# Optimization experiments

Measured on AMD Instinct MI355X. Metric: run time of the kernel, lower is better.

The kernel has to match this reference:

```python
import jax, jax.numpy as jnp
import numpy as np
from math import factorial

B, C, D = 1024, 10, 16
EPS = 1e-07


def _moment_weights(dim, order):
    # weight[idx] = prod(multiplicity!)/order!  (de-duplicates symmetric index tuples)
    if order == 1:
        return np.ones((dim,), dtype=np.float32)
    grids = np.meshgrid(*([np.arange(dim)] * order), indexing='ij')
    idx = np.stack(grids, axis=-1)  # [dim]*order + [order]
    prodm = np.ones(idx.shape[:-1], dtype=np.float64)
    for p in range(order):
        r = np.ones(idx.shape[:-1], dtype=np.float64)
        for q in range(p):
            r += (idx[..., q] == idx[..., p])
        prodm *= r  # running multiplicities multiply to prod(m!)
    return (prodm / float(factorial(order))).astype(np.float32)


def _gauss_moments(dim, order):
    # joint moments of N(0, I) via Isserlis' theorem
    eye = np.eye(dim)
    if order == 1:
        return np.zeros((dim,), np.float32)
    if order == 2:
        return eye.astype(np.float32)
    if order == 3:
        return np.zeros((dim, dim, dim), np.float32)
    g = (np.einsum('ij,kl->ijkl', eye, eye)
         + np.einsum('ik,jl->ijkl', eye, eye)
         + np.einsum('il,jk->ijkl', eye, eye))
    return g.astype(np.float32)


def _sroot(x, c1, p, c2):
    # signed compressive root: sign(sign(x)+0.1) * ((|x|+c1)^p - c2)
    return jnp.sign(jnp.sign(x) + 0.1) * (jnp.power(jnp.abs(x) + c1, p) - c2)


def setup_inputs() -> dict:
    key = jax.random.key(0)
    k1, k2, k3 = jax.random.split(key, 3)
    return {
        'embedding': jax.random.normal(k1, (B, D), dtype=jnp.float32),
        'centers': jax.random.normal(k2, (C, D), dtype=jnp.float32),
        'logits': jax.random.normal(k3, (B, C), dtype=jnp.float32),
        'gm1': jnp.asarray(_gauss_moments(D, 1)),
        'gm2': jnp.asarray(_gauss_moments(D, 2)),
        'gm3': jnp.asarray(_gauss_moments(D, 3)),
        'gm4': jnp.asarray(_gauss_moments(D, 4)),
        'mw1': jnp.asarray(_moment_weights(D, 1)),
        'mw2': jnp.asarray(_moment_weights(D, 2)),
        'mw3': jnp.asarray(_moment_weights(D, 3)),
        'mw4': jnp.asarray(_moment_weights(D, 4)),
    }


def reference(embedding, centers, logits, gm1, gm2, gm3, gm4, mw1, mw2, mw3, mw4):
    num_classes = logits.shape[1]
    assign = jnp.argmax(logits, axis=-1)                      # [B]
    onehot = jax.nn.one_hot(assign, num_classes, dtype=embedding.dtype)  # [B,C]
    diff = embedding[:, None, :] - centers[None, :, :]        # [B,C,D]
    d = diff * onehot[:, :, None]                             # diff_onehot [B,C,D]
    cw = jnp.sum(onehot, axis=0)                              # cluster_weight [C]

    # fused moment contractions (original materializes [B,C,D^k] then sums over B;
    # onehot is 0/1 so onehot^k == onehot -> identical math)
    m1 = jnp.sum(d, axis=0) / (cw[:, None] + EPS)                             # [C,D]
    m2 = jnp.einsum('bci,bcj->cij', d, d) / (cw[:, None, None] + EPS)         # [C,D,D]
    m3 = jnp.einsum('bci,bcj,bck->cijk', d, d, d)                             # [C,D,D,D] (no count division, as in original)
    m4 = jnp.einsum('bci,bcj,bck,bcl->cijkl', d, d, d, d)                     # [C,D,D,D,D]

    m2 = _sroot(m2, 0.25, 0.5, 0.5)
    m3 = _sroot(m3, 0.19245008973, 0.3333333333, 0.57735026919)
    m4 = _sroot(m4, 0.15749013123, 0.25, 0.62996052494)
    t1 = gm1
    t2 = _sroot(gm2, 0.25, 0.5, 0.5)
    t3 = _sroot(gm3, 0.19245008973, 0.3333333333, 0.57735026919)
    t4 = _sroot(gm4, 0.15749013123, 0.25, 0.62996052494)

    cwn = cw / jnp.sum(cw)                                     # [C]
    w1 = cwn[:, None] * mw1[None, :]
    w2 = cwn[:, None, None] * mw2[None]
    w3 = cwn[:, None, None, None] * mw3[None]
    w4 = cwn[:, None, None, None, None] * mw4[None]

    p1 = jnp.sum(w1 * jnp.square(m1 - t1[None]))
    p2 = jnp.sum(w2 * jnp.square(m2 - t2[None]))
    p3 = jnp.sum(w3 * jnp.square(m3 - t3[None]))
    p4 = jnp.sum(w4 * jnp.square(m4 - t4[None]))
    return 1.0 * p1 + 0.5 * p2 + 0.25 * p3 + 0.125 * p4
```

## Files before the change

### kernel.cpp

```cpp
#include <hip/hip_runtime.h>
#include <math.h>

#define BN 1024
#define CN 10
#define DN 16
#define NE1 16
#define NE2 136
#define NE3 816
#define NE4 3876
#define NENT 4844
#define EB 19
#define CH 256
#define EPSV 1e-7f

__device__ __forceinline__ int H2f(int n){ return n*(n+1)/2; }
__device__ __forceinline__ int H3f(int n){ return n*(n+1)*(n+2)/6; }

__device__ __forceinline__ float sroot2f(float x){
  float s = (x<0.f)?-1.f:1.f;
  return s*(sqrtf(fabsf(x)+0.25f)-0.5f);
}
__device__ __forceinline__ float sroot3f(float x){
  float s=(x<0.f)?-1.f:1.f;
  return s*(cbrtf(fabsf(x)+0.19245008973f)-0.57735026919f);
}
__device__ __forceinline__ float sroot4f(float x){
  float s=(x<0.f)?-1.f:1.f;
  return s*(sqrtf(sqrtf(fabsf(x)+0.15749013123f))-0.62996052494f);
}

__global__ __launch_bounds__(1024) void ka(
    const float* __restrict__ logits,
    int* __restrict__ counts, int* __restrict__ idxlist,
    float* __restrict__ acc, int* __restrict__ ticket) {
  int tid  = threadIdx.x;
  int lane = tid & 63;
  int wave = tid >> 6;
  if (tid == 0) { acc[0] = 0.f; ticket[0] = 0; }

  const float* lr = logits + tid*CN;
  float best = lr[0]; int bi = 0;
  #pragma unroll
  for (int c=1;c<CN;c++){ float v=lr[c]; if (v>best){best=v;bi=c;} }

  __shared__ int wcnt[16][CN];
  int lanerank = 0;
  #pragma unroll
  for (int c=0;c<CN;c++){
    unsigned long long m = __ballot(bi==c);
    if (bi==c) lanerank = __popcll(m & ((1ull<<lane)-1ull));
    if (lane==0) wcnt[wave][c] = __popcll(m);
  }
  __syncthreads();
  int off = 0;
  for (int w=0; w<wave; w++) off += wcnt[w][bi];
  idxlist[bi*BN + off + lanerank] = tid;

  if (tid < CN) {
    int t = 0;
    #pragma unroll
    for (int w=0; w<16; w++) t += wcnt[w][tid];
    counts[tid] = t;
  }
}

__global__ __launch_bounds__(256) void kb(
    const float* __restrict__ emb, const float* __restrict__ centers,
    const float* __restrict__ gm1, const float* __restrict__ gm2,
    const float* __restrict__ gm3, const float* __restrict__ gm4,
    const int* __restrict__ counts, const int* __restrict__ idxlist,
    float* __restrict__ acc, int* __restrict__ ticket,
    float* __restrict__ out) {
  __shared__ float sx[17][CH+1];
  __shared__ float red[256];
  int tid = threadIdx.x;
  int c  = blockIdx.x / EB;
  int eb = blockIdx.x % EB;
  int cnt = counts[c];

  for (int n=tid; n<CH+1; n+=256) sx[16][n] = 1.f;

  int e = eb*256 + tid;
  int ii=16, jj=16, kk=16, ll=16, order=1;
  float tg = 0.f;
  bool valid = (e < NENT);
  if (valid) {
    if (e < NE1) {
      order=1; ii=e;
      tg = gm1[ii];
    } else if (e < NE1+NE2) {
      order=2; int r = e-NE1;
      int i=0; while (r >= DN-i){ r -= DN-i; i++; }
      ii=i; jj=i+r;
      tg = sroot2f(gm2[ii*DN+jj]);
    } else if (e < NE1+NE2+NE3) {
      order=3; int r = e-(NE1+NE2);
      int i=0; while (r >= H2f(DN-i)){ r -= H2f(DN-i); i++; }
      int j=i; while (r >= DN-j){ r -= DN-j; j++; }
      ii=i; jj=j; kk=j+r;
      tg = sroot3f(gm3[(ii*DN+jj)*DN+kk]);
    } else {
      order=4; int r = e-(NE1+NE2+NE3);
      int i=0; while (r >= H3f(DN-i)){ r -= H3f(DN-i); i++; }
      int j=i; while (r >= H2f(DN-j)){ r -= H2f(DN-j); j++; }
      int k=j; while (r >= DN-k){ r -= DN-k; k++; }
      ii=i; jj=j; kk=k; ll=k+r;
      tg = sroot4f(gm4[((ii*DN+jj)*DN+kk)*DN+ll]);
    }
  }

  float mom = 0.f;
  for (int base=0; base<cnt; base+=CH) {
    int m = min(CH, cnt-base);
    __syncthreads();
    if (tid < m) {
      int b = idxlist[c*BN + base + tid];
      const float4* er = (const float4*)(emb + b*DN);
      const float4* cr = (const float4*)(centers + c*DN);
      float4 e0=er[0], e1=er[1], e2=er[2], e3=er[3];
      float4 c0=cr[0], c1=cr[1], c2=cr[2], c3=cr[3];
      float v[16];
      v[0]=e0.x-c0.x; v[1]=e0.y-c0.y; v[2]=e0.z-c0.z; v[3]=e0.w-c0.w;
      v[4]=e1.x-c1.x; v[5]=e1.y-c1.y; v[6]=e1.z-c1.z; v[7]=e1.w-c1.w;
      v[8]=e2.x-c2.x; v[9]=e2.y-c2.y; v[10]=e2.z-c2.z; v[11]=e2.w-c2.w;
      v[12]=e3.x-c3.x; v[13]=e3.y-c3.y; v[14]=e3.z-c3.z; v[15]=e3.w-c3.w;
      #pragma unroll
      for (int i=0;i<16;i++) sx[i][tid] = v[i];
    }
    __syncthreads();
    for (int n=0; n<m; n++) {
      mom += sx[ii][n]*sx[jj][n]*sx[kk][n]*sx[ll][n];
    }
  }

  float contrib = 0.f;
  if (valid) {
    float mval = mom;
    if (order <= 2) mval /= ((float)cnt + EPSV);
    float v;
    if      (order==1) v = mval - tg;
    else if (order==2) v = sroot2f(mval) - tg;
    else if (order==3) v = sroot3f(mval) - tg;
    else               v = sroot4f(mval) - tg;
    float lw = (order==1)?1.f:(order==2)?0.5f:(order==3)?0.25f:0.125f;
    float cwn = (float)cnt * (1.f/1024.f);
    contrib = lw * cwn * v * v;
  }

  red[tid] = contrib;
  __syncthreads();
  for (int s=128; s>0; s>>=1) {
    if (tid < s) red[tid] += red[tid+s];
    __syncthreads();
  }
  if (tid==0) {
    atomicAdd(acc, red[0]);
    __threadfence();
    int old = atomicAdd(ticket, 1);
    if (old == (int)gridDim.x - 1) {
      float total = atomicAdd(acc, 0.0f);
      out[0] = total;
    }
  }
}

extern "C" void kernel_launch(void* const* d_in, const int* in_sizes, int n_in,
                              void* d_out, int out_size, void* d_ws, size_t ws_size,
                              hipStream_t stream) {
  const float* emb  = (const float*)d_in[0];
  const float* cen  = (const float*)d_in[1];
  const float* logi = (const float*)d_in[2];
  const float* gm1  = (const float*)d_in[3];
  const float* gm2  = (const float*)d_in[4];
  const float* gm3  = (const float*)d_in[5];
  const float* gm4  = (const float*)d_in[6];

  int*   counts  = (int*)d_ws;
  int*   idxlist = counts + CN;
  float* acc     = (float*)(idxlist + CN*BN);
  int*   ticket  = (int*)(acc + 1);

  ka<<<1, 1024, 0, stream>>>(logi, counts, idxlist, acc, ticket);
  kb<<<CN*EB, 256, 0, stream>>>(emb, cen, gm1, gm2, gm3, gm4,
                                counts, idxlist, acc, ticket, (float*)d_out);
}
```

Measured before the change: 20.59 us.

## Fuse argmax bucketing into moment kernel and drop ticket-based final reduction

```diff
diff --git a/kernel.cpp b/kernel.cpp
--- a/kernel.cpp
+++ b/kernel.cpp
@@ -29,56 +29,45 @@
   return s*(sqrtf(sqrtf(fabsf(x)+0.15749013123f))-0.62996052494f);
 }
 
-__global__ __launch_bounds__(1024) void ka(
+__global__ __launch_bounds__(256) void kb(
+    const float* __restrict__ emb, const float* __restrict__ centers,
     const float* __restrict__ logits,
-    int* __restrict__ counts, int* __restrict__ idxlist,
-    float* __restrict__ acc, int* __restrict__ ticket) {
+    const float* __restrict__ gm1, const float* __restrict__ gm2,
+    const float* __restrict__ gm3, const float* __restrict__ gm4,
+    float* __restrict__ out) {
+  __shared__ float sx[17][CH+1];
+  __shared__ float red[256];
+  __shared__ int   memb[BN];
+  __shared__ int   wcnt[4][4];
   int tid  = threadIdx.x;
   int lane = tid & 63;
   int wave = tid >> 6;
-  if (tid == 0) { acc[0] = 0.f; ticket[0] = 0; }
+  int c  = blockIdx.x / EB;
+  int eb = blockIdx.x % EB;
 
-  const float* lr = logits + tid*CN;
-  float best = lr[0]; int bi = 0;
+  for (int n=tid; n<CH+1; n+=256) sx[16][n] = 1.f;
+
+  int rank_r[4]; bool match_r[4];
   #pragma unroll
-  for (int c=1;c<CN;c++){ float v=lr[c]; if (v>best){best=v;bi=c;} }
-
-  __shared__ int wcnt[16][CN];
-  int lanerank = 0;
-  #pragma unroll
-  for (int c=0;c<CN;c++){
+  for (int r=0;r<4;r++) {
+    int b = r*256 + tid;
+    const float* lr = logits + b*CN;
+    float best = lr[0]; int bi = 0;
+    #pragma unroll
+    for (int q=1;q<CN;q++){ float v=lr[q]; if (v>best){best=v;bi=q;} }
     unsigned long long m = __ballot(bi==c);
-    if (bi==c) lanerank = __popcll(m & ((1ull<<lane)-1ull));
-    if (lane==0) wcnt[wave][c] = __popcll(m);
+    match_r[r] = (bi==c);
+    rank_r[r] = __popcll(m & ((1ull<<lane)-1ull));
+    if (lane==0) wcnt[r][wave] = __popcll(m);
   }
   __syncthreads();
-  int off = 0;
-  for (int w=0; w<wave; w++) off += wcnt[w][bi];
-  idxlist[bi*BN + off + lanerank] = tid;
-
-  if (tid < CN) {
-    int t = 0;
-    #pragma unroll
-    for (int w=0; w<16; w++) t += wcnt[w][tid];
-    counts[tid] = t;
-  }
-}
-
-__global__ __launch_bounds__(256) void kb(
-    const float* __restrict__ emb, const float* __restrict__ centers,
-    const float* __restrict__ gm1, const float* __restrict__ gm2,
-    const float* __restrict__ gm3, const float* __restrict__ gm4,
-    const int* __restrict__ counts, const int* __restrict__ idxlist,
-    float* __restrict__ acc, int* __restrict__ ticket,
-    float* __restrict__ out) {
-  __shared__ float sx[17][CH+1];
-  __shared__ float red[256];
-  int tid = threadIdx.x;
-  int c  = blockIdx.x / EB;
-  int eb = blockIdx.x % EB;
-  int cnt = counts[c];
-
-  for (int n=tid; n<CH+1; n+=256) sx[16][n] = 1.f;
+  int pre[17]; pre[0]=0;
+  #pragma unroll
+  for (int p=0;p<16;p++) pre[p+1] = pre[p] + wcnt[p>>2][p&3];
+  int cnt = pre[16];
+  #pragma unroll
+  for (int r=0;r<4;r++)
+    if (match_r[r]) memb[pre[r*4+wave] + rank_r[r]] = r*256 + tid;
 
   int e = eb*256 + tid;
   int ii=16, jj=16, kk=16, ll=16, order=1;
@@ -114,7 +103,7 @@
     int m = min(CH, cnt-base);
     __syncthreads();
     if (tid < m) {
-      int b = idxlist[c*BN + base + tid];
+      int b = memb[base + tid];
       const float4* er = (const float4*)(emb + b*DN);
       const float4* cr = (const float4*)(centers + c*DN);
       float4 e0=er[0], e1=er[1], e2=er[2], e3=er[3];
@@ -153,15 +142,7 @@
     if (tid < s) red[tid] += red[tid+s];
     __syncthreads();
   }
-  if (tid==0) {
-    atomicAdd(acc, red[0]);
-    __threadfence();
-    int old = atomicAdd(ticket, 1);
-    if (old == (int)gridDim.x - 1) {
-      float total = atomicAdd(acc, 0.0f);
-      out[0] = total;
-    }
-  }
+  if (tid==0) atomicAdd(out, red[0]);
 }
 
 extern "C" void kernel_launch(void* const* d_in, const int* in_sizes, int n_in,
@@ -175,12 +156,6 @@
   const float* gm3  = (const float*)d_in[5];
   const float* gm4  = (const float*)d_in[6];
 
-  int*   counts  = (int*)d_ws;
-  int*   idxlist = counts + CN;
-  float* acc     = (float*)(idxlist + CN*BN);
-  int*   ticket  = (int*)(acc + 1);
-
-  ka<<<1, 1024, 0, stream>>>(logi, counts, idxlist, acc, ticket);
-  kb<<<CN*EB, 256, 0, stream>>>(emb, cen, gm1, gm2, gm3, gm4,
-                                counts, idxlist, acc, ticket, (float*)d_out);
+  hipMemsetAsync(d_out, 0, sizeof(float), stream);
+  kb<<<CN*EB, 256, 0, stream>>>(emb, cen, logi, gm1, gm2, gm3, gm4, (float*)d_out);
 }
```

Measured after the change: 18.99 us. 1.08x faster.
